# Kernel tuning notes

Hardware: AMD Instinct MI355X
Metric: run time of the kernel (lower is better)

Reference implementation:

```python
import jax, jax.numpy as jnp
import numpy as np

B, L, DIM, S, K = 2, 2048, 1024, 16, 3
INNER = DIM  # expand = 1 (module only runs with expand=1, see notes)


def setup_inputs() -> dict:
    key = jax.random.key(0)
    ks = jax.random.split(key, 10)
    f = lambda k, shape, s=0.02: jax.random.normal(k, shape, jnp.float32) * s
    return {
        "x": jax.random.normal(ks[0], (B, L, DIM), jnp.float32),
        "gamma": jnp.ones((DIM,), jnp.float32),
        "beta": jnp.zeros((DIM,), jnp.float32),
        "W_in": f(ks[1], (2 * INNER, DIM)),
        "conv_w": f(ks[2], (INNER, 1, K), 0.2),   # depthwise conv, OIL layout
        "W_x": f(ks[3], (2 * S, INNER)),
        "W_dt": f(ks[4], (INNER, DIM)),
        "b_dt": f(ks[5], (INNER,), 0.1),
        "A_log": jax.random.normal(ks[6], (INNER, S), jnp.float32),
        "D_param": jnp.ones((INNER,), jnp.float32),
        "W_out": f(ks[7], (DIM, INNER)),
    }


def reference(x, gamma, beta, W_in, conv_w, W_x, W_dt, b_dt, A_log, D_param, W_out):
    residual = x
    # LayerNorm
    mu = jnp.mean(x, axis=-1, keepdims=True)
    var = jnp.var(x, axis=-1, keepdims=True)
    h = (x - mu) / jnp.sqrt(var + 1e-5) * gamma + beta
    # in_proj + chunk
    xz = jnp.einsum('bld,ed->ble', h, W_in)
    inner = W_in.shape[0] // 2
    xx, z = xz[..., :inner], xz[..., inner:]
    # depthwise conv1d, padding (K-1)//2, no bias
    k = conv_w.shape[-1]
    pad = (k - 1) // 2
    xc = jax.lax.conv_general_dilated(
        xx.transpose(0, 2, 1), conv_w, window_strides=(1,),
        padding=[(pad, pad)], dimension_numbers=('NCL', 'OIL', 'NCL'),
        feature_group_count=inner).transpose(0, 2, 1)
    xc = jax.nn.silu(xc)
    # projections for dt, B, C
    dt = jnp.einsum('bld,ed->ble', xc, W_dt) + b_dt
    BC = jnp.einsum('bld,ed->ble', xc, W_x)
    s = A_log.shape[-1]
    Bm, Cm = BC[..., :s], BC[..., s:]
    # selective scan
    A = -jnp.exp(A_log)                               # (d, s)
    dt = jax.nn.softplus(dt)                          # (b, l, d)
    dA = jnp.exp(jnp.einsum('bld,ds->blds', dt, A))   # (b, l, d, s)
    dB = jnp.einsum('bld,bls->blds', dt, Bm)          # (b, l, d, s)

    def step(state, inputs):
        dA_t, dB_t, C_t = inputs                      # (b,d,s), (b,d,s), (b,s)
        state = state * dA_t + dB_t
        y_t = jnp.einsum('bds,bs->bd', state, C_t)
        return state, y_t

    init = jnp.zeros((x.shape[0], inner, s), xc.dtype)
    _, ys = jax.lax.scan(
        step, init,
        (dA.transpose(1, 0, 2, 3), dB.transpose(1, 0, 2, 3), Cm.transpose(1, 0, 2)))
    y = ys.transpose(1, 0, 2)                         # (b, l, d)
    # skip, gate, out projection, residual
    y = y + D_param * xc
    y = y * jax.nn.silu(z)
    out = jnp.einsum('bld,ed->ble', y, W_out)
    return out + residual
```

## Files before the change

kernel.cpp:

```cpp
#include <hip/hip_runtime.h>
#include <math.h>

#define BB 2
#define LL 2048
#define DIMV 1024
#define SSV 16
#define INNERV 1024
#define E2V 2048
#define MMV (BB*LL)
#define NCHUNK 64
#define CLEN 32

typedef __attribute__((ext_vector_type(8))) short short8;
typedef __attribute__((ext_vector_type(4))) float f32x4;

static __device__ __forceinline__ float4 ld4(const float* p){
  return *reinterpret_cast<const float4*>(p);
}
static __device__ __forceinline__ ushort f2bf(float x){
  unsigned u = __float_as_uint(x);
  unsigned r = (u + 0x7fffu + ((u >> 16) & 1u)) >> 16;
  return (ushort)r;
}
static __device__ __forceinline__ float bf2f(ushort h){
  return __uint_as_float(((unsigned)h) << 16);
}
static __device__ __forceinline__ void gld16(const void* g, void* l){
  __builtin_amdgcn_global_load_lds(
      (const __attribute__((address_space(1))) void*)g,
      (__attribute__((address_space(3))) void*)l, 16, 0, 0);
}

__global__ __launch_bounds__(256) void ln_init(
        const float* __restrict__ x, const float* __restrict__ gamma,
        const float* __restrict__ beta, ushort* __restrict__ hh,
        const float* __restrict__ W_in, const float* __restrict__ W_dt,
        const float* __restrict__ W_out, const float* __restrict__ wx,
        ushort* __restrict__ Wih, ushort* __restrict__ Wdh,
        ushort* __restrict__ Woh, float* __restrict__ wxt){
  __shared__ float red[8];
  if (blockIdx.x < 4224){
    int idx = blockIdx.x*256 + threadIdx.x;
    if (idx < 1024*1024){
      const float* src; ushort* dst; int i;
      if (idx < 512*1024){ src = W_in;  dst = Wih; i = idx; }
      else if (idx < 768*1024){ src = W_dt;  dst = Wdh; i = idx - 512*1024; }
      else { src = W_out; dst = Woh; i = idx - 768*1024; }
      float4 v = ld4(src + (size_t)i*4);
      ushort4 H;
      H.x=f2bf(v.x); H.y=f2bf(v.y); H.z=f2bf(v.z); H.w=f2bf(v.w);
      *reinterpret_cast<ushort4*>(dst + (size_t)i*4) = H;
    } else {
      int j = idx - 1024*1024;
      int e = j >> 10, k = j & 1023;
      wxt[k*32 + e] = wx[j];
    }
    return;
  }
  int row = blockIdx.x - 4224;
  int tid = threadIdx.x;
  const float* xr = x + (size_t)row*DIMV;
  float4 v = ld4(xr + tid*4);
  float s  = v.x+v.y+v.z+v.w;
  float s2 = v.x*v.x+v.y*v.y+v.z*v.z+v.w*v.w;
  for (int o=32;o;o>>=1){ s += __shfl_down(s,o); s2 += __shfl_down(s2,o); }
  int wid = tid>>6, lane = tid&63;
  if (lane==0){ red[wid]=s; red[4+wid]=s2; }
  __syncthreads();
  s  = red[0]+red[1]+red[2]+red[3];
  s2 = red[4]+red[5]+red[6]+red[7];
  float mu  = s*(1.f/DIMV);
  float var = s2*(1.f/DIMV) - mu*mu;
  float rstd = rsqrtf(var + 1e-5f);
  float4 g = ld4(gamma + tid*4), be = ld4(beta + tid*4);
  ushort4 H;
  H.x = f2bf((v.x-mu)*rstd*g.x + be.x);
  H.y = f2bf((v.y-mu)*rstd*g.y + be.y);
  H.z = f2bf((v.z-mu)*rstd*g.z + be.z);
  H.w = f2bf((v.w-mu)*rstd*g.w + be.w);
  *reinterpret_cast<ushort4*>(hh + (size_t)row*DIMV + tid*4) = H;
}

#define GBK 64
#define NKT 16

template<int EPI, int BN>
static __device__ __forceinline__ void gemm_body(ushort* lds,
    const ushort* __restrict__ A, const ushort* __restrict__ Bw,
    void* __restrict__ Co_, int N, const float* __restrict__ aux,
    int bm, int bn){
  const int t  = threadIdx.x;

  const int rr  = t >> 3;
  const int k16 = (t & 7) ^ (rr & 7);
  const ushort* gA = A  + (size_t)(bm + rr)*1024 + k16*8;
  const ushort* gB = Bw + (size_t)(bn + rr)*1024 + k16*8;
  const int wofs = (t >> 6) * 1024;

  const int l  = t & 63, wv = t >> 6;
  const int wm = wv & 1, wn = wv >> 1;
  const int fr = l & 15, kb = l >> 4;
  const int WN = BN/2;
  const int NF = BN/64;

  f32x4 acc[4][2*NF];
  #pragma unroll
  for (int m=0;m<4;m++){
    #pragma unroll
    for (int n=0;n<2*NF;n++) acc[m][n] = (f32x4){0.f,0.f,0.f,0.f};
  }

  char* Lb = (char*)lds;
  for (int kt = 0; kt < NKT; ++kt){
    const int ko = kt*GBK;
    gld16(gA + ko,           Lb +     0 + wofs);
    gld16(gA + ko + 32*1024, Lb +  4096 + wofs);
    gld16(gA + ko + 64*1024, Lb +  8192 + wofs);
    gld16(gA + ko + 96*1024, Lb + 12288 + wofs);
    gld16(gB + ko,           Lb + 16384 + wofs);
    gld16(gB + ko + 32*1024, Lb + 20480 + wofs);
    if (BN == 128){
      gld16(gB + ko + 64*1024, Lb + 24576 + wofs);
      gld16(gB + ko + 96*1024, Lb + 28672 + wofs);
    }
    __syncthreads();
    short8 a[4][2], b[2*NF][2];
    #pragma unroll
    for (int m=0;m<4;m++){
      int row = wm*64 + m*16 + fr;
      #pragma unroll
      for (int ks=0;ks<2;ks++)
        a[m][ks] = *(const short8*)(Lb + row*128 + (((ks*4+kb)^(fr&7))*16));
    }
    #pragma unroll
    for (int n=0;n<2*NF;n++){
      int row = wn*WN + n*16 + fr;
      #pragma unroll
      for (int ks=0;ks<2;ks++)
        b[n][ks] = *(const short8*)(Lb + 16384 + row*128 + (((ks*4+kb)^(fr&7))*16));
    }
    #pragma unroll
    for (int ks=0;ks<2;ks++){
      #pragma unroll
      for (int m=0;m<4;m++){
        #pragma unroll
        for (int n=0;n<2*NF;n++)
          acc[m][n] = __builtin_amdgcn_mfma_f32_16x16x32_bf16(a[m][ks], b[n][ks], acc[m][n], 0,0,0);
      }
    }
    __syncthreads();
  }

  #pragma unroll
  for (int m=0;m<4;m++){
    int row0 = bm + wm*64 + m*16 + kb*4;
    #pragma unroll
    for (int n=0;n<2*NF;n++){
      int col = bn + wn*WN + n*16 + fr;
      #pragma unroll
      for (int j=0;j<4;j++){
        int r = row0 + j;
        float v = acc[m][n][j];
        if (EPI==0){
          ((ushort*)Co_)[(size_t)r*N + col] = f2bf(v);
        } else if (EPI==1){
          v += aux[col];
          v = (v > 20.f) ? v : log1pf(__expf(v));
          ((ushort*)Co_)[(size_t)r*N + col] = f2bf(v);
        } else {
          v += aux[(size_t)r*N + col];
          ((float*)Co_)[(size_t)r*N + col] = v;
        }
      }
    }
  }
}

template<int EPI, int BN>
__global__ __launch_bounds__(256) void gemm_bf16(
    const ushort* __restrict__ A, const ushort* __restrict__ Bw,
    void* __restrict__ Co_, int N, const float* __restrict__ aux){
  __shared__ __align__(16) ushort lds[(128+BN)*GBK];
  gemm_body<EPI,BN>(lds, A, Bw, Co_, N, aux, blockIdx.y*128, blockIdx.x*BN);
}

static __device__ __forceinline__ void bc_body(ushort* sh,
    const ushort* __restrict__ xch, const float* __restrict__ wxt,
    float* __restrict__ bc, int blk){
  int tid = threadIdx.x;
  int row0 = blk * 8;
  const ushort4* srcH = (const ushort4*)(xch + (size_t)row0*DIMV);
  #pragma unroll
  for (int i=0;i<8;i++)
    ((ushort4*)sh)[tid + i*256] = srcH[tid + i*256];
  __syncthreads();
  int r = tid >> 5, e = tid & 31;
  float acc = 0.f;
  for (int k=0;k<1024;k++){
    acc = fmaf(bf2f(sh[r*1024+k]), wxt[k*32+e], acc);
  }
  bc[(size_t)(row0 + r)*32 + e] = acc;
}

__global__ __launch_bounds__(256) void gemm1_bc(
    const ushort* __restrict__ xch, const ushort* __restrict__ Wdh,
    ushort* __restrict__ dtb, const float* __restrict__ b_dt,
    const float* __restrict__ wxt, float* __restrict__ bcb){
  __shared__ __align__(16) ushort lds[(128+64)*GBK];
  if (blockIdx.y < 32){
    gemm_body<1,64>(lds, xch, Wdh, dtb, INNERV, b_dt, blockIdx.y*128, blockIdx.x*64);
  } else {
    bc_body(lds, xch, wxt, bcb, (blockIdx.y-32)*16 + blockIdx.x);
  }
}

__global__ __launch_bounds__(256) void conv_silu_kernel(const ushort* __restrict__ xz,
        const float* __restrict__ cw, ushort* __restrict__ xch){
  int idx = blockIdx.x*256 + threadIdx.x;
  int d4  = idx & 255;
  int row = idx >> 8;
  int t = row & (LL-1);
  const ushort* p = xz + (size_t)row*E2V + d4*4;
  ushort4 u1 = *reinterpret_cast<const ushort4*>(p);
  ushort4 u0 = (t>0)    ? *reinterpret_cast<const ushort4*>(p - E2V) : make_ushort4(0,0,0,0);
  ushort4 u2 = (t<LL-1) ? *reinterpret_cast<const ushort4*>(p + E2V) : make_ushort4(0,0,0,0);
  int d = d4*4;
  float w[12];
  #pragma unroll
  for (int i=0;i<12;i++) w[i] = cw[d*3 + i];
  float4 o;
  o.x = bf2f(u0.x)*w[0] + bf2f(u1.x)*w[1]  + bf2f(u2.x)*w[2];
  o.y = bf2f(u0.y)*w[3] + bf2f(u1.y)*w[4]  + bf2f(u2.y)*w[5];
  o.z = bf2f(u0.z)*w[6] + bf2f(u1.z)*w[7]  + bf2f(u2.z)*w[8];
  o.w = bf2f(u0.w)*w[9] + bf2f(u1.w)*w[10] + bf2f(u2.w)*w[11];
  o.x = o.x / (1.f + __expf(-o.x));
  o.y = o.y / (1.f + __expf(-o.y));
  o.z = o.z / (1.f + __expf(-o.z));
  o.w = o.w / (1.f + __expf(-o.w));
  ushort4 H;
  H.x=f2bf(o.x); H.y=f2bf(o.y); H.z=f2bf(o.z); H.w=f2bf(o.w);
  *reinterpret_cast<ushort4*>(xch + (size_t)row*DIMV + d4*4) = H;
}

__global__ __launch_bounds__(256) void scan_p1(const ushort* __restrict__ dt,
        const float* __restrict__ bc, const float* __restrict__ A_log,
        float* __restrict__ F, float* __restrict__ P){
  __shared__ float sB[CLEN*32];
  int bid = blockIdx.x;
  int dblk = bid & 3;
  int c  = (bid >> 2) & (NCHUNK-1);
  int b  = bid >> 8;
  int tid = threadIdx.x;
  int d = dblk*256 + tid;
  int row0 = b*LL + c*CLEN;
  ((float4*)sB)[tid] = *((const float4*)(bc + (size_t)row0*32) + tid);
  float a[16];
  {
    const float4* ap = (const float4*)(A_log + d*16);
    #pragma unroll
    for (int q=0;q<4;q++){
      float4 v = ap[q];
      a[q*4+0]=-__expf(v.x); a[q*4+1]=-__expf(v.y);
      a[q*4+2]=-__expf(v.z); a[q*4+3]=-__expf(v.w);
    }
  }
  __syncthreads();
  float st[16];
  #pragma unroll
  for (int s=0;s<16;s++) st[s]=0.f;
  float sdt = 0.f;
  const ushort* dtp = dt + (size_t)row0*DIMV + d;
  for (int t=0;t<CLEN;t++){
    float dtv = bf2f(dtp[(size_t)t*DIMV]);
    sdt += dtv;
    float4 B0 = *(const float4*)&sB[t*32+0];
    float4 B1 = *(const float4*)&sB[t*32+4];
    float4 B2 = *(const float4*)&sB[t*32+8];
    float4 B3 = *(const float4*)&sB[t*32+12];
    float Bv[16] = {B0.x,B0.y,B0.z,B0.w,B1.x,B1.y,B1.z,B1.w,
                    B2.x,B2.y,B2.z,B2.w,B3.x,B3.y,B3.z,B3.w};
    #pragma unroll
    for (int s=0;s<16;s++){
      float dA = __expf(dtv*a[s]);
      st[s] = fmaf(st[s], dA, dtv*Bv[s]);
    }
  }
  size_t o = ((size_t)((b*NCHUNK + c)*DIMV + d))*16;
  #pragma unroll
  for (int q=0;q<4;q++){
    *(float4*)(F + o + q*4) = make_float4(st[q*4],st[q*4+1],st[q*4+2],st[q*4+3]);
    *(float4*)(P + o + q*4) = make_float4(__expf(sdt*a[q*4]),  __expf(sdt*a[q*4+1]),
                                          __expf(sdt*a[q*4+2]),__expf(sdt*a[q*4+3]));
  }
}

__global__ __launch_bounds__(256) void scan_p2(const float* __restrict__ F,
        const float* __restrict__ P, float* __restrict__ E){
  int idx = blockIdx.x*256 + threadIdx.x;
  int b  = idx >> 14;
  int ds = idx & 16383;
  float e = 0.f;
  for (int c=0;c<NCHUNK;c++){
    size_t o = ((size_t)(b*NCHUNK + c) << 14) + ds;
    E[o] = e;
    e = fmaf(P[o], e, F[o]);
  }
}

__global__ __launch_bounds__(256) void scan_p3(const ushort* __restrict__ dt,
        const float* __restrict__ bc, const float* __restrict__ A_log,
        const float* __restrict__ E, const ushort* __restrict__ xch,
        const ushort* __restrict__ xz, const float* __restrict__ Dp,
        ushort* __restrict__ yh){
  __shared__ float sBC[CLEN*32];
  int bid = blockIdx.x;
  int dblk = bid & 3;
  int c  = (bid >> 2) & (NCHUNK-1);
  int b  = bid >> 8;
  int tid = threadIdx.x;
  int d = dblk*256 + tid;
  int row0 = b*LL + c*CLEN;
  ((float4*)sBC)[tid] = *((const float4*)(bc + (size_t)row0*32) + tid);
  float a[16];
  {
    const float4* ap = (const float4*)(A_log + d*16);
    #pragma unroll
    for (int q=0;q<4;q++){
      float4 v = ap[q];
      a[q*4+0]=-__expf(v.x); a[q*4+1]=-__expf(v.y);
      a[q*4+2]=-__expf(v.z); a[q*4+3]=-__expf(v.w);
    }
  }
  float st[16];
  {
    size_t o = ((size_t)((b*NCHUNK + c)*DIMV + d))*16;
    #pragma unroll
    for (int q=0;q<4;q++){
      float4 v = *(const float4*)(E + o + q*4);
      st[q*4]=v.x; st[q*4+1]=v.y; st[q*4+2]=v.z; st[q*4+3]=v.w;
    }
  }
  float Dv = Dp[d];
  __syncthreads();
  const ushort* dtp = dt + (size_t)row0*DIMV + d;
  for (int t=0;t<CLEN;t++){
    float dtv = bf2f(dtp[(size_t)t*DIMV]);
    float4 B0 = *(const float4*)&sBC[t*32+0];
    float4 B1 = *(const float4*)&sBC[t*32+4];
    float4 B2 = *(const float4*)&sBC[t*32+8];
    float4 B3 = *(const float4*)&sBC[t*32+12];
    float4 C0 = *(const float4*)&sBC[t*32+16];
    float4 C1 = *(const float4*)&sBC[t*32+20];
    float4 C2 = *(const float4*)&sBC[t*32+24];
    float4 C3 = *(const float4*)&sBC[t*32+28];
    float Bv[16] = {B0.x,B0.y,B0.z,B0.w,B1.x,B1.y,B1.z,B1.w,
                    B2.x,B2.y,B2.z,B2.w,B3.x,B3.y,B3.z,B3.w};
    float Cv[16] = {C0.x,C0.y,C0.z,C0.w,C1.x,C1.y,C1.z,C1.w,
                    C2.x,C2.y,C2.z,C2.w,C3.x,C3.y,C3.z,C3.w};
    float y = 0.f;
    #pragma unroll
    for (int s=0;s<16;s++){
      float dA = __expf(dtv*a[s]);
      st[s] = fmaf(st[s], dA, dtv*Bv[s]);
      y = fmaf(st[s], Cv[s], y);
    }
    int row = row0 + t;
    size_t ofs = (size_t)row*DIMV + d;
    float xcv = bf2f(xch[ofs]);
    float zv  = bf2f(xz[(size_t)row*E2V + INNERV + d]);
    float sz  = zv / (1.f + __expf(-zv));
    yh[ofs] = f2bf((y + Dv*xcv)*sz);
  }
}

extern "C" void kernel_launch(void* const* d_in, const int* in_sizes, int n_in,
                              void* d_out, int out_size, void* d_ws, size_t ws_size,
                              hipStream_t stream){
  const float* x     = (const float*)d_in[0];
  const float* gamma = (const float*)d_in[1];
  const float* beta  = (const float*)d_in[2];
  const float* W_in  = (const float*)d_in[3];
  const float* cw    = (const float*)d_in[4];
  const float* W_x   = (const float*)d_in[5];
  const float* W_dt  = (const float*)d_in[6];
  const float* b_dt  = (const float*)d_in[7];
  const float* A_log = (const float*)d_in[8];
  const float* Dp    = (const float*)d_in[9];
  const float* W_out = (const float*)d_in[10];
  float* out = (float*)d_out;
  float* ws  = (float*)d_ws;
  const size_t MB = (size_t)1 << 20;
  ushort* xzh = (ushort*)ws;
  ushort* hh  = (ushort*)(ws + 4*MB);
  ushort* yh  = (ushort*)(ws + 4*MB);
  ushort* xch = (ushort*)(ws + 6*MB);
  ushort* dtb = (ushort*)(ws + 8*MB);
  float*  F   = ws + 10*MB;
  float*  P   = ws + 12*MB;
  float*  E   = ws + 14*MB;
  ushort* Wih = (ushort*)(ws + 16*MB);
  ushort* Wdh = (ushort*)(ws + 17*MB);
  ushort* Woh = (ushort*)(ws + 17*MB + 512*1024);
  float*  bcb = ws + 18*MB;
  float*  wxt = ws + 18*MB + 128*1024;

  ln_init<<<4224 + MMV, 256, 0, stream>>>(x, gamma, beta, hh,
                                          W_in, W_dt, W_out, W_x,
                                          Wih, Wdh, Woh, wxt);
  gemm_bf16<0,128><<<dim3(E2V/128, MMV/128), 256, 0, stream>>>(hh, Wih, xzh, E2V, nullptr);
  conv_silu_kernel<<<(MMV*(DIMV/4))/256, 256, 0, stream>>>(xzh, cw, xch);
  gemm1_bc<<<dim3(16, 64), 256, 0, stream>>>(xch, Wdh, dtb, b_dt, wxt, bcb);
  scan_p1<<<BB*NCHUNK*(DIMV/256), 256, 0, stream>>>(dtb, bcb, A_log, F, P);
  scan_p2<<<(BB*DIMV*SSV)/256, 256, 0, stream>>>(F, P, E);
  scan_p3<<<BB*NCHUNK*(DIMV/256), 256, 0, stream>>>(dtb, bcb, A_log, E, xch, xzh, Dp, yh);
  gemm_bf16<2,64><<<dim3(DIMV/64, MMV/128), 256, 0, stream>>>(yh, Woh, out, DIMV, x);
}
```

Baseline: 160.8 us.

## Split fused dt/BC kernel and stage W_x tiles in LDS for BC projection

The fused gemm1_bc launch, which ran the dt GEMM and the B/C projection as different block roles, is split into two separate launches. The BC projection becomes its own kernel that stages 128-row slices of the transposed W_x into shared memory and uses four independent accumulators over vectorized bf16 loads, instead of reading weights from global memory one element at a time. This is meant to shorten the long serial per-thread dot products that could leave the fused kernel's BC blocks as stragglers. In exchange it adds a kernel launch and loses the concurrency the fused grid provided.

```diff
diff --git a/kernel.cpp b/kernel.cpp
--- a/kernel.cpp
+++ b/kernel.cpp
@@ -85,11 +85,12 @@
 #define NKT 16
 
 template<int EPI, int BN>
-static __device__ __forceinline__ void gemm_body(ushort* lds,
+__global__ __launch_bounds__(256) void gemm_bf16(
     const ushort* __restrict__ A, const ushort* __restrict__ Bw,
-    void* __restrict__ Co_, int N, const float* __restrict__ aux,
-    int bm, int bn){
+    void* __restrict__ Co_, int N, const float* __restrict__ aux){
+  __shared__ __align__(16) ushort lds[(128+BN)*GBK];
   const int t  = threadIdx.x;
+  const int bm = blockIdx.y * 128, bn = blockIdx.x * BN;
 
   const int rr  = t >> 3;
   const int k16 = (t & 7) ^ (rr & 7);
@@ -176,42 +177,36 @@
   }
 }
 
-template<int EPI, int BN>
-__global__ __launch_bounds__(256) void gemm_bf16(
-    const ushort* __restrict__ A, const ushort* __restrict__ Bw,
-    void* __restrict__ Co_, int N, const float* __restrict__ aux){
-  __shared__ __align__(16) ushort lds[(128+BN)*GBK];
-  gemm_body<EPI,BN>(lds, A, Bw, Co_, N, aux, blockIdx.y*128, blockIdx.x*BN);
-}
-
-static __device__ __forceinline__ void bc_body(ushort* sh,
-    const ushort* __restrict__ xch, const float* __restrict__ wxt,
-    float* __restrict__ bc, int blk){
+__global__ __launch_bounds__(256) void bc_kernel(const ushort* __restrict__ xch,
+        const float* __restrict__ wxt, float* __restrict__ bc){
+  __shared__ ushort sh[8*1024];
+  __shared__ float  sw[128*32];
   int tid = threadIdx.x;
-  int row0 = blk * 8;
+  int row0 = blockIdx.x * 8;
   const ushort4* srcH = (const ushort4*)(xch + (size_t)row0*DIMV);
   #pragma unroll
   for (int i=0;i<8;i++)
     ((ushort4*)sh)[tid + i*256] = srcH[tid + i*256];
-  __syncthreads();
   int r = tid >> 5, e = tid & 31;
-  float acc = 0.f;
-  for (int k=0;k<1024;k++){
-    acc = fmaf(bf2f(sh[r*1024+k]), wxt[k*32+e], acc);
-  }
-  bc[(size_t)(row0 + r)*32 + e] = acc;
-}
-
-__global__ __launch_bounds__(256) void gemm1_bc(
-    const ushort* __restrict__ xch, const ushort* __restrict__ Wdh,
-    ushort* __restrict__ dtb, const float* __restrict__ b_dt,
-    const float* __restrict__ wxt, float* __restrict__ bcb){
-  __shared__ __align__(16) ushort lds[(128+64)*GBK];
-  if (blockIdx.y < 32){
-    gemm_body<1,64>(lds, xch, Wdh, dtb, INNERV, b_dt, blockIdx.y*128, blockIdx.x*64);
-  } else {
-    bc_body(lds, xch, wxt, bcb, (blockIdx.y-32)*16 + blockIdx.x);
-  }
+  float a0=0.f, a1=0.f, a2=0.f, a3=0.f;
+  for (int kt=0; kt<8; ++kt){
+    __syncthreads();
+    const float4* wsrc = (const float4*)(wxt + kt*128*32);
+    #pragma unroll
+    for (int i=0;i<4;i++)
+      ((float4*)sw)[tid + i*256] = wsrc[tid + i*256];
+    __syncthreads();
+    const ushort* xr = &sh[r*1024 + kt*128];
+    #pragma unroll
+    for (int k=0;k<128;k+=4){
+      ushort4 xv = *(const ushort4*)&xr[k];
+      a0 = fmaf(bf2f(xv.x), sw[(k+0)*32+e], a0);
+      a1 = fmaf(bf2f(xv.y), sw[(k+1)*32+e], a1);
+      a2 = fmaf(bf2f(xv.z), sw[(k+2)*32+e], a2);
+      a3 = fmaf(bf2f(xv.w), sw[(k+3)*32+e], a3);
+    }
+  }
+  bc[(size_t)(row0 + r)*32 + e] = (a0+a1)+(a2+a3);
 }
 
 __global__ __launch_bounds__(256) void conv_silu_kernel(const ushort* __restrict__ xz,
@@ -409,7 +404,8 @@
                                           Wih, Wdh, Woh, wxt);
   gemm_bf16<0,128><<<dim3(E2V/128, MMV/128), 256, 0, stream>>>(hh, Wih, xzh, E2V, nullptr);
   conv_silu_kernel<<<(MMV*(DIMV/4))/256, 256, 0, stream>>>(xzh, cw, xch);
-  gemm1_bc<<<dim3(16, 64), 256, 0, stream>>>(xch, Wdh, dtb, b_dt, wxt, bcb);
+  gemm_bf16<1,64><<<dim3(INNERV/64, MMV/128), 256, 0, stream>>>(xch, Wdh, dtb, INNERV, b_dt);
+  bc_kernel<<<MMV/8, 256, 0, stream>>>(xch, wxt, bcb);
   scan_p1<<<BB*NCHUNK*(DIMV/256), 256, 0, stream>>>(dtb, bcb, A_log, F, P);
   scan_p2<<<(BB*DIMV*SSV)/256, 256, 0, stream>>>(F, P, E);
   scan_p3<<<BB*NCHUNK*(DIMV/256), 256, 0, stream>>>(dtb, bcb, A_log, E, xch, xzh, Dp, yh);
```

Result: slower. 167.7 us (+4.3%).
